# Optimization experiments

Measured on AMD Instinct MI355X. Metric: run time of the kernel, lower is better.

## Reference

```python
import jax, jax.numpy as jnp
import numpy as np

B, N, DIM, H = 8, 1024, 768, 12
DH = DIM // H          # 64
LATENT = 32
EPS = 1e-5


def setup_inputs() -> dict:
    key = jax.random.key(0)
    ks = jax.random.split(key, 6)
    s = 0.02
    return {
        "x": jax.random.normal(ks[0], (B, N, DIM), jnp.float32),
        "Wq": jax.random.normal(ks[1], (DIM, DIM), jnp.float32) * s,
        "Wkv": jax.random.normal(ks[2], (DIM, DIM), jnp.float32) * s,
        "Wo_ctx": jax.random.normal(ks[3], (DIM, DIM), jnp.float32) * s,
        "bo_ctx": jnp.zeros((DIM,), jnp.float32),
        "Wo_lat": jax.random.normal(ks[4], (DIM, DIM), jnp.float32) * s,
        "bo_lat": jnp.zeros((DIM,), jnp.float32),
        "ln_g": jnp.ones((DH,), jnp.float32),
        "ln_b": jnp.zeros((DH,), jnp.float32),
    }


def _heads(t):
    # 'b n (h d) -> (b h) n d'
    b, n, _ = t.shape
    return t.reshape(b, n, H, DH).transpose(0, 2, 1, 3).reshape(b * H, n, DH)


def _merge(t, b):
    # '(b h) n d -> b n (h d)'
    _, n, dh = t.shape
    return t.reshape(b, H, n, dh).transpose(0, 2, 1, 3).reshape(b, n, H * dh)


def _ln(v, g, bta):
    mu = v.mean(-1, keepdims=True)
    var = ((v - mu) ** 2).mean(-1, keepdims=True)
    return (v - mu) * jax.lax.rsqrt(var + EPS) * g + bta


def _rope(t):
    # rotary embedding over full head dim (lucidrains-style half rotation)
    n, dh = t.shape[-2], t.shape[-1]
    inv = 1.0 / (10000.0 ** (jnp.arange(0, dh, 2, dtype=jnp.float32) / dh))
    f = jnp.arange(n, dtype=jnp.float32)[:, None] * inv[None, :]   # [n, dh/2]
    f = jnp.concatenate([f, f], -1)[None]                          # [1, n, dh]
    x1, x2 = jnp.split(t, 2, -1)
    rot = jnp.concatenate([-x2, x1], -1)
    return t * jnp.cos(f) + rot * jnp.sin(f)


def reference(x, Wq, Wkv, Wo_ctx, bo_ctx, Wo_lat, bo_lat, ln_g, ln_b):
    b, n, _ = x.shape
    ctx = n - LATENT  # context_len
    q = _heads(x @ Wq)
    kv = _heads(x @ Wkv)
    # layer_num == 0: rotary applied to both q and kv
    q = _rope(q)
    kv = _rope(kv)
    q = q * (DH ** -0.5)
    q_lat, q_ctx = q[:, ctx:], q[:, :ctx]
    kv_ctx = kv[:, :ctx]
    lkv = _ln(kv, ln_g, ln_b)
    lkv_ctx = _ln(kv_ctx, ln_g, ln_b)
    # latent queries attend to ALL positions; context attends to context only
    attn_lat = jax.nn.softmax(jnp.einsum('bid,bkd->bik', q_lat, kv), axis=-1)
    attn_ctx = jax.nn.softmax(jnp.einsum('bid,bkd->bik', q_ctx, kv_ctx), axis=-1)
    out_lat = _merge(jnp.einsum('bik,bkd->bid', attn_lat, lkv), b) @ Wo_lat + bo_lat
    out_ctx = _merge(jnp.einsum('bik,bkd->bid', attn_ctx, lkv_ctx), b) @ Wo_ctx + bo_ctx
    return jnp.concatenate([out_ctx, out_lat], axis=1)  # [b, n, dim]
```

## Files before the change

### kernel.cpp

```cpp
#include <hip/hip_runtime.h>

#define B_    8
#define N_    1024
#define DIM_  768
#define H_    12
#define DH_   64
#define CTX_  992
#define BH_   (B_ * H_)
#define EPS_  1e-5f
#define WSZ_  (DIM_ * DIM_)
#define PS_   72

typedef unsigned short ush;
typedef __attribute__((ext_vector_type(8))) short bf8_t;
typedef __attribute__((ext_vector_type(4))) float f4_t;

__device__ __forceinline__ float b2f(ush u) {
    return __uint_as_float(((unsigned)u) << 16);
}
__device__ __forceinline__ ush f2b(float f) {
    unsigned u = __float_as_uint(f);
    u += 0x7fffu + ((u >> 16) & 1u);
    return (ush)(u >> 16);
}
__device__ __forceinline__ void gload_lds16(const void* g, void* l) {
    __builtin_amdgcn_global_load_lds(
        (const __attribute__((address_space(1))) void*)g,
        (__attribute__((address_space(3))) void*)l, 16, 0, 0);
}

__global__ __launch_bounds__(256) void cast_all(
    const float* __restrict__ X, ush* __restrict__ Xb,
    const float* __restrict__ W0, const float* __restrict__ W1,
    const float* __restrict__ W2, const float* __restrict__ W3,
    ush* __restrict__ T0, ush* __restrict__ T1,
    ush* __restrict__ T2, ush* __restrict__ T3)
{
    __shared__ ush T[64][65];
    const int bid = blockIdx.x;
    const int tid = threadIdx.x;

    if (bid < 6144) {
        const int i4 = bid * 256 + tid;
        float4 v = *(const float4*)&X[(size_t)i4 * 4];
        ushort4 o;
        o.x = f2b(v.x); o.y = f2b(v.y); o.z = f2b(v.z); o.w = f2b(v.w);
        *(ushort4*)&Xb[(size_t)i4 * 4] = o;
        return;
    }
    const int t = bid - 6144;
    const int z = t / 144, rem = t % 144;
    const int i0 = (rem / 12) * 64;
    const int j0 = (rem % 12) * 64;
    const float* W = (z == 0) ? W0 : (z == 1) ? W1 : (z == 2) ? W2 : W3;
    ush* Wt        = (z == 0) ? T0 : (z == 1) ? T1 : (z == 2) ? T2 : T3;

    const int r4 = tid >> 4, c = (tid & 15) << 2;
    #pragma unroll
    for (int g = 0; g < 4; ++g) {
        const int r = r4 + g * 16;
        float4 v = *(const float4*)&W[(size_t)(i0 + r) * DIM_ + j0 + c];
        T[r][c + 0] = f2b(v.x); T[r][c + 1] = f2b(v.y);
        T[r][c + 2] = f2b(v.z); T[r][c + 3] = f2b(v.w);
    }
    __syncthreads();
    const int nl = tid >> 2, k0l = (tid & 3) << 4;
    #pragma unroll
    for (int g = 0; g < 4; ++g) {
        ushort4 o;
        o.x = T[k0l + 4 * g + 0][nl]; o.y = T[k0l + 4 * g + 1][nl];
        o.z = T[k0l + 4 * g + 2][nl]; o.w = T[k0l + 4 * g + 3][nl];
        *(ushort4*)&Wt[(size_t)(j0 + nl) * DIM_ + i0 + k0l + 4 * g] = o;
    }
}

__global__ __launch_bounds__(256, 3) void gemm_qkv_mfma(
    const ush* __restrict__ Xb, const ush* __restrict__ Wt0,
    const ush* __restrict__ Wt1, ush* __restrict__ Q16, ush* __restrict__ K16,
    ush* __restrict__ Vn, const float* __restrict__ ln_g,
    const float* __restrict__ ln_b)
{
    const int z   = blockIdx.z;
    const ush* Bt = z ? Wt1 : Wt0;
    const int m0 = blockIdx.y * 128, c0 = blockIdx.x * 128;
    const int tid = threadIdx.x;
    const int w = tid >> 6, lane = tid & 63, l15 = lane & 15, quad = lane >> 4;
    const int wm = w >> 1, wn = w & 1;

    __shared__ __align__(16) ush As[128 * 32];
    __shared__ __align__(16) ush Bs[128 * 32];

    const int slot0 = w * 2 * 64 + lane;
    const int srow0 = slot0 >> 2, scc0 = (slot0 & 3) ^ (srow0 & 3);
    const int slot1 = slot0 + 64;
    const int srow1 = slot1 >> 2, scc1 = (slot1 & 3) ^ (srow1 & 3);

    f4_t acc[4][4];
    #pragma unroll
    for (int i = 0; i < 4; ++i)
        #pragma unroll
        for (int j = 0; j < 4; ++j)
            #pragma unroll
            for (int r = 0; r < 4; ++r) acc[i][j][r] = 0.f;

    for (int k0 = 0; k0 < DIM_; k0 += 32) {
        __syncthreads();
        gload_lds16((const char*)Xb + (size_t)(m0 + srow0) * (DIM_ * 2) + k0 * 2 + scc0 * 16,
                    (char*)As + slot0 * 16);
        gload_lds16((const char*)Bt + (size_t)(c0 + srow0) * (DIM_ * 2) + k0 * 2 + scc0 * 16,
                    (char*)Bs + slot0 * 16);
        gload_lds16((const char*)Xb + (size_t)(m0 + srow1) * (DIM_ * 2) + k0 * 2 + scc1 * 16,
                    (char*)As + slot1 * 16);
        gload_lds16((const char*)Bt + (size_t)(c0 + srow1) * (DIM_ * 2) + k0 * 2 + scc1 * 16,
                    (char*)Bs + slot1 * 16);
        __syncthreads();

        const int sq = (quad ^ (l15 & 3)) * 8;
        bf8_t af[4];
        #pragma unroll
        for (int mi = 0; mi < 4; ++mi)
            af[mi] = *(const bf8_t*)&As[(wm * 64 + mi * 16 + l15) * 32 + sq];
        #pragma unroll
        for (int ni = 0; ni < 4; ++ni) {
            bf8_t bfr = *(const bf8_t*)&Bs[(wn * 64 + ni * 16 + l15) * 32 + sq];
            #pragma unroll
            for (int mi = 0; mi < 4; ++mi)
                acc[mi][ni] = __builtin_amdgcn_mfma_f32_16x16x32_bf16(
                    af[mi], bfr, acc[mi][ni], 0, 0, 0);
        }
    }

    const float inv0 = __expf(-(float)l15 * (9.210340371976184f / 32.0f));
    const float inv1 = inv0 * 0.01f;
    const int h  = (c0 >> 6) + wn;
    const int b  = (m0 + wm * 64) >> 10;
    const int nb = (m0 + wm * 64) & 1023;

    #pragma unroll
    for (int mi = 0; mi < 4; ++mi) {
        #pragma unroll
        for (int r = 0; r < 4; ++r) {
            const int n = nb + mi * 16 + quad * 4 + r;
            float sn0, cs0, sn1, cs1;
            __sincosf((float)n * inv0, &sn0, &cs0);
            __sincosf((float)n * inv1, &sn1, &cs1);
            {
                float a = acc[mi][0][r], p = acc[mi][2][r];
                acc[mi][0][r] = a * cs0 - p * sn0;
                acc[mi][2][r] = p * cs0 + a * sn0;
            }
            {
                float a = acc[mi][1][r], p = acc[mi][3][r];
                acc[mi][1][r] = a * cs1 - p * sn1;
                acc[mi][3][r] = p * cs1 + a * sn1;
            }
        }
    }

    if (z == 0) {
        #pragma unroll
        for (int mi = 0; mi < 4; ++mi)
            #pragma unroll
            for (int ni = 0; ni < 4; ++ni)
                #pragma unroll
                for (int r = 0; r < 4; ++r) {
                    const int n = nb + mi * 16 + quad * 4 + r;
                    const int d = ni * 16 + l15;
                    Q16[(((size_t)b * H_ + h) * N_ + n) * DH_ + d] =
                        f2b(acc[mi][ni][r] * 0.125f);
                }
    } else {
        float g4[4], b4[4];
        #pragma unroll
        for (int ni = 0; ni < 4; ++ni) {
            g4[ni] = ln_g[ni * 16 + l15];
            b4[ni] = ln_b[ni * 16 + l15];
        }
        #pragma unroll
        for (int mi = 0; mi < 4; ++mi)
            #pragma unroll
            for (int r = 0; r < 4; ++r) {
                const int n = nb + mi * 16 + quad * 4 + r;
                const size_t rowoff = (((size_t)b * H_ + h) * N_ + n) * DH_;
                float s = (acc[mi][0][r] + acc[mi][1][r]) +
                          (acc[mi][2][r] + acc[mi][3][r]);
                #pragma unroll
                for (int o = 8; o >= 1; o >>= 1) s += __shfl_xor(s, o);
                const float mu = s * (1.0f / 64.0f);
                float sq = 0.f;
                #pragma unroll
                for (int ni = 0; ni < 4; ++ni) {
                    const float dv = acc[mi][ni][r] - mu;
                    sq = fmaf(dv, dv, sq);
                }
                #pragma unroll
                for (int o = 8; o >= 1; o >>= 1) sq += __shfl_xor(sq, o);
                const float rstd = rsqrtf(sq * (1.0f / 64.0f) + EPS_);
                #pragma unroll
                for (int ni = 0; ni < 4; ++ni) {
                    const int d = ni * 16 + l15;
                    K16[rowoff + d] = f2b(acc[mi][ni][r]);
                    Vn[rowoff + d]  = f2b((acc[mi][ni][r] - mu) * rstd * g4[ni] + b4[ni]);
                }
            }
    }
}

__global__ __launch_bounds__(256) void transpose_v(
    const ush* __restrict__ Vn, ush* __restrict__ Vt)
{
    const int bh = blockIdx.y;
    const int n0 = blockIdx.x * 64;
    const int tid = threadIdx.x;

    __shared__ ush T[64][65];

    const int r4 = tid >> 4, c = (tid & 15) << 2;
    #pragma unroll
    for (int g = 0; g < 4; ++g) {
        const int r = r4 + g * 16;
        ushort4 v = *(const ushort4*)&Vn[((size_t)bh * N_ + n0 + r) * DH_ + c];
        T[r][c + 0] = v.x; T[r][c + 1] = v.y; T[r][c + 2] = v.z; T[r][c + 3] = v.w;
    }
    __syncthreads();
    const int dl = tid >> 2, G0 = (tid & 3) << 2;
    #pragma unroll
    for (int g = 0; g < 4; ++g) {
        const int G = G0 + g;
        ushort4 o;
        o.x = T[G][dl]; o.y = T[16 + G][dl];
        o.z = T[32 + G][dl]; o.w = T[48 + G][dl];
        *(ushort4*)&Vt[((size_t)bh * DH_ + dl) * N_ + n0 + 4 * G] = o;
    }
}

__global__ __launch_bounds__(256, 4) void attn_mfma(
    const ush* __restrict__ Qh, const ush* __restrict__ Kh,
    const ush* __restrict__ Vt, ush* __restrict__ ATT)
{
    const int bh = blockIdx.x % BH_;
    const int q0 = (blockIdx.x / BH_) * 128;
    const int tid = threadIdx.x;
    const int w = tid >> 6, lane = tid & 63, l15 = lane & 15, quad = lane >> 4;

    __shared__ __align__(16) ush Ks[64 * 64];
    __shared__ __align__(16) ush Vs[64 * 64];
    __shared__ __align__(16) ush QPs[128 * PS_];

    const int sw8 = (l15 & 7);

    {
        const char* qg = (const char*)(Qh + ((size_t)bh * N_ + q0) * DH_);
        #pragma unroll
        for (int i = 0; i < 4; ++i) {
            const int slot = (w * 4 + i) * 64 + lane;
            const int row = slot >> 3, cc = (slot & 7) ^ (row & 7);
            gload_lds16(qg + (size_t)row * 128 + cc * 16, (char*)QPs + slot * 16);
        }
    }
    __syncthreads();

    bf8_t aq[2][2];
    #pragma unroll
    for (int mi = 0; mi < 2; ++mi)
        #pragma unroll
        for (int ks = 0; ks < 2; ++ks)
            aq[mi][ks] = *(const bf8_t*)&QPs[(w * 32 + mi * 16 + l15) * 64 +
                                             (((ks * 4 + quad) ^ sw8) * 8)];

    f4_t O[2][4];
    float l_[2][4];
    #pragma unroll
    for (int mi = 0; mi < 2; ++mi)
        #pragma unroll
        for (int r = 0; r < 4; ++r) {
            l_[mi][r] = 0.f;
            #pragma unroll
            for (int ni = 0; ni < 4; ++ni) O[mi][ni][r] = 0.f;
        }

    const char* kg = (const char*)(Kh + (size_t)bh * N_ * DH_);
    const char* vg = (const char*)(Vt + (size_t)bh * DH_ * N_);

    for (int t = 0; t < 16; ++t) {
        __syncthreads();
        #pragma unroll
        for (int i = 0; i < 2; ++i) {
            const int slot = (w * 2 + i) * 64 + lane;
            const int row = slot >> 3, cc = (slot & 7) ^ (row & 7);
            gload_lds16(kg + (size_t)(t * 64 + row) * 128 + cc * 16,
                        (char*)Ks + slot * 16);
            gload_lds16(vg + (size_t)row * (N_ * 2) + t * 128 + cc * 16,
                        (char*)Vs + slot * 16);
        }
        __syncthreads();

        f4_t s[2][4];
        #pragma unroll
        for (int mi = 0; mi < 2; ++mi)
            #pragma unroll
            for (int ni = 0; ni < 4; ++ni)
                #pragma unroll
                for (int r = 0; r < 4; ++r) s[mi][ni][r] = 0.f;
        #pragma unroll
        for (int ks = 0; ks < 2; ++ks)
            #pragma unroll
            for (int ni = 0; ni < 4; ++ni) {
                bf8_t bk = *(const bf8_t*)&Ks[(ni * 16 + l15) * 64 +
                                              (((ks * 4 + quad) ^ sw8) * 8)];
                #pragma unroll
                for (int mi = 0; mi < 2; ++mi)
                    s[mi][ni] = __builtin_amdgcn_mfma_f32_16x16x32_bf16(
                        aq[mi][ks], bk, s[mi][ni], 0, 0, 0);
            }

        if (t == 15) {
            #pragma unroll
            for (int mi = 0; mi < 2; ++mi)
                #pragma unroll
                for (int r = 0; r < 4; ++r) {
                    const int row = q0 + w * 32 + mi * 16 + quad * 4 + r;
                    if (row < CTX_) { s[mi][2][r] = -1e30f; s[mi][3][r] = -1e30f; }
                }
        }

        #pragma unroll
        for (int mi = 0; mi < 2; ++mi)
            #pragma unroll
            for (int r = 0; r < 4; ++r) {
                float p0 = __expf(s[mi][0][r]), p1 = __expf(s[mi][1][r]);
                float p2 = __expf(s[mi][2][r]), p3 = __expf(s[mi][3][r]);
                l_[mi][r] += (p0 + p1) + (p2 + p3);
                ushort4 pk;
                pk.x = f2b(p0); pk.y = f2b(p1); pk.z = f2b(p2); pk.w = f2b(p3);
                *(ushort4*)&QPs[(w * 32 + mi * 16 + quad * 4 + r) * PS_ + l15 * 4] = pk;
            }

        #pragma unroll
        for (int ks = 0; ks < 2; ++ks) {
            bf8_t ap[2];
            #pragma unroll
            for (int mi = 0; mi < 2; ++mi)
                ap[mi] = *(const bf8_t*)&QPs[(w * 32 + mi * 16 + l15) * PS_ +
                                             ks * 32 + quad * 8];
            #pragma unroll
            for (int ni = 0; ni < 4; ++ni) {
                bf8_t bv = *(const bf8_t*)&Vs[(ni * 16 + l15) * 64 +
                                              (((ks * 4 + quad) ^ sw8) * 8)];
                #pragma unroll
                for (int mi = 0; mi < 2; ++mi)
                    O[mi][ni] = __builtin_amdgcn_mfma_f32_16x16x32_bf16(
                        ap[mi], bv, O[mi][ni], 0, 0, 0);
            }
        }
    }

    const int b = bh / H_, h = bh % H_;
    #pragma unroll
    for (int mi = 0; mi < 2; ++mi)
        #pragma unroll
        for (int r = 0; r < 4; ++r) {
            float l = l_[mi][r];
            #pragma unroll
            for (int o = 8; o >= 1; o >>= 1) l += __shfl_xor(l, o);
            const float inv = 1.0f / l;
            const int row = q0 + w * 32 + mi * 16 + quad * 4 + r;
            #pragma unroll
            for (int ni = 0; ni < 4; ++ni)
                ATT[((size_t)b * N_ + row) * DIM_ + h * DH_ + ni * 16 + l15] =
                    f2b(O[mi][ni][r] * inv);
        }
}

__global__ __launch_bounds__(256, 2) void gemm_o_mfma(
    const ush* __restrict__ ATT, const ush* __restrict__ Btc,
    const float* __restrict__ biasc, const ush* __restrict__ Btl,
    const float* __restrict__ biasl, float* __restrict__ out)
{
    const int lat = (blockIdx.y >= 64);
    const ush* Bt     = lat ? Btl : Btc;
    const float* bias = lat ? biasl : biasc;
    const int m0 = (lat ? (blockIdx.y - 64) : blockIdx.y) * 128;
    const int c0 = blockIdx.x * 128;
    const int tid = threadIdx.x;
    const int w = tid >> 6, lane = tid & 63, l15 = lane & 15, quad = lane >> 4;
    const int wm = w >> 1, wn = w & 1;

    __shared__ __align__(16) ush As[128 * 32];
    __shared__ __align__(16) ush Bs[128 * 32];

    const int slot0 = w * 2 * 64 + lane;
    const int srow0 = slot0 >> 2, scc0 = (slot0 & 3) ^ (srow0 & 3);
    const int slot1 = slot0 + 64;
    const int srow1 = slot1 >> 2, scc1 = (slot1 & 3) ^ (srow1 & 3);
    const int am0 = m0 + srow0, am1 = m0 + srow1;
    const int grow0 = lat ? (((am0 >> 5) << 10) + CTX_ + (am0 & 31)) : am0;
    const int grow1 = lat ? (((am1 >> 5) << 10) + CTX_ + (am1 & 31)) : am1;

    f4_t acc[4][4];
    #pragma unroll
    for (int i = 0; i < 4; ++i)
        #pragma unroll
        for (int j = 0; j < 4; ++j)
            #pragma unroll
            for (int r = 0; r < 4; ++r) acc[i][j][r] = 0.f;

    for (int k0 = 0; k0 < DIM_; k0 += 32) {
        __syncthreads();
        gload_lds16((const char*)ATT + (size_t)grow0 * (DIM_ * 2) + k0 * 2 + scc0 * 16,
                    (char*)As + slot0 * 16);
        gload_lds16((const char*)Bt + (size_t)(c0 + srow0) * (DIM_ * 2) + k0 * 2 + scc0 * 16,
                    (char*)Bs + slot0 * 16);
        gload_lds16((const char*)ATT + (size_t)grow1 * (DIM_ * 2) + k0 * 2 + scc1 * 16,
                    (char*)As + slot1 * 16);
        gload_lds16((const char*)Bt + (size_t)(c0 + srow1) * (DIM_ * 2) + k0 * 2 + scc1 * 16,
                    (char*)Bs + slot1 * 16);
        __syncthreads();

        const int sq = (quad ^ (l15 & 3)) * 8;
        bf8_t af[4];
        #pragma unroll
        for (int mi = 0; mi < 4; ++mi)
            af[mi] = *(const bf8_t*)&As[(wm * 64 + mi * 16 + l15) * 32 + sq];
        #pragma unroll
        for (int ni = 0; ni < 4; ++ni) {
            bf8_t bfr = *(const bf8_t*)&Bs[(wn * 64 + ni * 16 + l15) * 32 + sq];
            #pragma unroll
            for (int mi = 0; mi < 4; ++mi)
                acc[mi][ni] = __builtin_amdgcn_mfma_f32_16x16x32_bf16(
                    af[mi], bfr, acc[mi][ni], 0, 0, 0);
        }
    }

    #pragma unroll
    for (int mi = 0; mi < 4; ++mi)
        #pragma unroll
        for (int ni = 0; ni < 4; ++ni) {
            const int c = c0 + wn * 64 + ni * 16 + l15;
            const float bs = bias[c];
            #pragma unroll
            for (int r = 0; r < 4; ++r) {
                const int m = m0 + wm * 64 + mi * 16 + quad * 4 + r;
                if (!lat && (m & 1023) >= CTX_) continue;
                const int grow = lat ? (((m >> 5) << 10) + CTX_ + (m & 31)) : m;
                out[(size_t)grow * DIM_ + c] = acc[mi][ni][r] + bs;
            }
        }
}

extern "C" void kernel_launch(void* const* d_in, const int* in_sizes, int n_in,
                              void* d_out, int out_size, void* d_ws, size_t ws_size,
                              hipStream_t stream) {
    const float* X      = (const float*)d_in[0];
    const float* Wq     = (const float*)d_in[1];
    const float* Wkv    = (const float*)d_in[2];
    const float* Wo_ctx = (const float*)d_in[3];
    const float* bo_ctx = (const float*)d_in[4];
    const float* Wo_lat = (const float*)d_in[5];
    const float* bo_lat = (const float*)d_in[6];
    const float* ln_g   = (const float*)d_in[7];
    const float* ln_b   = (const float*)d_in[8];
    float* out = (float*)d_out;

    ush* ws = (ush*)d_ws;
    const size_t E = (size_t)BH_ * N_ * DH_;
    ush* Xb  = ws;
    ush* Q16 = ws + E;
    ush* K16 = ws + 2 * E;
    ush* Vn  = ws + 3 * E;
    ush* Vt  = ws + 4 * E;
    ush* Wt0 = ws + 5 * E;
    ush* Wt1 = Wt0 + WSZ_;
    ush* Wt2 = Wt1 + WSZ_;
    ush* Wt3 = Wt2 + WSZ_;
    ush* ATT = Xb;

    cast_all<<<dim3(6144 + 576), 256, 0, stream>>>(X, Xb, Wq, Wkv, Wo_ctx,
                                                   Wo_lat, Wt0, Wt1, Wt2, Wt3);
    gemm_qkv_mfma<<<dim3(6, 64, 2), 256, 0, stream>>>(Xb, Wt0, Wt1, Q16, K16,
                                                      Vn, ln_g, ln_b);
    transpose_v<<<dim3(16, BH_), 256, 0, stream>>>(Vn, Vt);
    attn_mfma<<<dim3(8 * BH_), 256, 0, stream>>>(Q16, K16, Vt, ATT);
    gemm_o_mfma<<<dim3(6, 66), 256, 0, stream>>>(ATT, Wt2, bo_ctx, Wt3, bo_lat, out);
}
```

Baseline: 197.8 us.

## Fuse V transpose into QKV GEMM epilogue and use exp2 softmax

The layer-normed V tile is now written transposed through an enlarged shared-memory buffer in the QKV GEMM epilogue and stored directly as Vt. This removes the separate transpose kernel and the global round trip of the intermediate Vn. The Q scale now folds in log2(e) so attention can use exp2f instead of __expf. The shared tile grows to 128x136 bf16 and adds two barriers in the epilogue, which may lower occupancy of the GEMM.

```diff
diff --git a/kernel.cpp b/kernel.cpp
--- a/kernel.cpp
+++ b/kernel.cpp
@@ -10,6 +10,7 @@
 #define EPS_  1e-5f
 #define WSZ_  (DIM_ * DIM_)
 #define PS_   72
+#define VS_   136
 
 typedef unsigned short ush;
 typedef __attribute__((ext_vector_type(8))) short bf8_t;
@@ -77,7 +78,7 @@
 __global__ __launch_bounds__(256, 3) void gemm_qkv_mfma(
     const ush* __restrict__ Xb, const ush* __restrict__ Wt0,
     const ush* __restrict__ Wt1, ush* __restrict__ Q16, ush* __restrict__ K16,
-    ush* __restrict__ Vn, const float* __restrict__ ln_g,
+    ush* __restrict__ Vt, const float* __restrict__ ln_g,
     const float* __restrict__ ln_b)
 {
     const int z   = blockIdx.z;
@@ -87,8 +88,9 @@
     const int w = tid >> 6, lane = tid & 63, l15 = lane & 15, quad = lane >> 4;
     const int wm = w >> 1, wn = w & 1;
 
-    __shared__ __align__(16) ush As[128 * 32];
-    __shared__ __align__(16) ush Bs[128 * 32];
+    __shared__ __align__(16) ush SMEM[128 * VS_];
+    ush* As = SMEM;
+    ush* Bs = SMEM + 4096;
 
     const int slot0 = w * 2 * 64 + lane;
     const int srow0 = slot0 >> 2, scc0 = (slot0 & 3) ^ (srow0 & 3);
@@ -167,7 +169,7 @@
                     const int n = nb + mi * 16 + quad * 4 + r;
                     const int d = ni * 16 + l15;
                     Q16[(((size_t)b * H_ + h) * N_ + n) * DH_ + d] =
-                        f2b(acc[mi][ni][r] * 0.125f);
+                        f2b(acc[mi][ni][r] * 0.1803368801111731f);
                 }
     } else {
         float g4[4], b4[4];
@@ -176,6 +178,7 @@
             g4[ni] = ln_g[ni * 16 + l15];
             b4[ni] = ln_b[ni * 16 + l15];
         }
+        __syncthreads();
         #pragma unroll
         for (int mi = 0; mi < 4; ++mi)
             #pragma unroll
@@ -196,41 +199,25 @@
                 #pragma unroll
                 for (int o = 8; o >= 1; o >>= 1) sq += __shfl_xor(sq, o);
                 const float rstd = rsqrtf(sq * (1.0f / 64.0f) + EPS_);
+                const int np = wm * 64 + quad * 16 + r * 4 + mi;
                 #pragma unroll
                 for (int ni = 0; ni < 4; ++ni) {
                     const int d = ni * 16 + l15;
                     K16[rowoff + d] = f2b(acc[mi][ni][r]);
-                    Vn[rowoff + d]  = f2b((acc[mi][ni][r] - mu) * rstd * g4[ni] + b4[ni]);
+                    SMEM[(wn * 64 + ni * 16 + l15) * VS_ + np] =
+                        f2b((acc[mi][ni][r] - mu) * rstd * g4[ni] + b4[ni]);
                 }
             }
-    }
-}
-
-__global__ __launch_bounds__(256) void transpose_v(
-    const ush* __restrict__ Vn, ush* __restrict__ Vt)
-{
-    const int bh = blockIdx.y;
-    const int n0 = blockIdx.x * 64;
-    const int tid = threadIdx.x;
-
-    __shared__ ush T[64][65];
-
-    const int r4 = tid >> 4, c = (tid & 15) << 2;
-    #pragma unroll
-    for (int g = 0; g < 4; ++g) {
-        const int r = r4 + g * 16;
-        ushort4 v = *(const ushort4*)&Vn[((size_t)bh * N_ + n0 + r) * DH_ + c];
-        T[r][c + 0] = v.x; T[r][c + 1] = v.y; T[r][c + 2] = v.z; T[r][c + 3] = v.w;
-    }
-    __syncthreads();
-    const int dl = tid >> 2, G0 = (tid & 3) << 2;
-    #pragma unroll
-    for (int g = 0; g < 4; ++g) {
-        const int G = G0 + g;
-        ushort4 o;
-        o.x = T[G][dl]; o.y = T[16 + G][dl];
-        o.z = T[32 + G][dl]; o.w = T[48 + G][dl];
-        *(ushort4*)&Vt[((size_t)bh * DH_ + dl) * N_ + n0 + 4 * G] = o;
+        __syncthreads();
+        const int bD  = ((m0 >> 10) * H_ + (c0 >> 6)) * 64;
+        const int nbb = m0 & 1023;
+        #pragma unroll
+        for (int i = 0; i < 8; ++i) {
+            const int chunk = tid + 256 * i;
+            const int cl = chunk >> 4, nc = (chunk & 15) * 8;
+            *(bf8_t*)&Vt[(size_t)(bD + cl) * N_ + nbb + nc] =
+                *(const bf8_t*)&SMEM[cl * VS_ + nc];
+        }
     }
 }
 
@@ -328,8 +315,8 @@
         for (int mi = 0; mi < 2; ++mi)
             #pragma unroll
             for (int r = 0; r < 4; ++r) {
-                float p0 = __expf(s[mi][0][r]), p1 = __expf(s[mi][1][r]);
-                float p2 = __expf(s[mi][2][r]), p3 = __expf(s[mi][3][r]);
+                float p0 = exp2f(s[mi][0][r]), p1 = exp2f(s[mi][1][r]);
+                float p2 = exp2f(s[mi][2][r]), p3 = exp2f(s[mi][3][r]);
                 l_[mi][r] += (p0 + p1) + (p2 + p3);
                 ushort4 pk;
                 pk.x = f2b(p0); pk.y = f2b(p1); pk.z = f2b(p2); pk.w = f2b(p3);
@@ -467,9 +454,8 @@
     ush* Xb  = ws;
     ush* Q16 = ws + E;
     ush* K16 = ws + 2 * E;
-    ush* Vn  = ws + 3 * E;
-    ush* Vt  = ws + 4 * E;
-    ush* Wt0 = ws + 5 * E;
+    ush* Vt  = ws + 3 * E;
+    ush* Wt0 = ws + 4 * E;
     ush* Wt1 = Wt0 + WSZ_;
     ush* Wt2 = Wt1 + WSZ_;
     ush* Wt3 = Wt2 + WSZ_;
@@ -478,8 +464,7 @@
     cast_all<<<dim3(6144 + 576), 256, 0, stream>>>(X, Xb, Wq, Wkv, Wo_ctx,
                                                    Wo_lat, Wt0, Wt1, Wt2, Wt3);
     gemm_qkv_mfma<<<dim3(6, 64, 2), 256, 0, stream>>>(Xb, Wt0, Wt1, Q16, K16,
-                                                      Vn, ln_g, ln_b);
-    transpose_v<<<dim3(16, BH_), 256, 0, stream>>>(Vn, Vt);
+                                                      Vt, ln_g, ln_b);
     attn_mfma<<<dim3(8 * BH_), 256, 0, stream>>>(Q16, K16, Vt, ATT);
     gemm_o_mfma<<<dim3(6, 66), 256, 0, stream>>>(ATT, Wt2, bo_ctx, Wt3, bo_lat, out);
 }
```

Measured after the change: 205.8 us. +4.0%, slower.
